# Optimization experiments

Measured on AMD Instinct MI355X. Metric: run time of the kernel, lower is better.

The kernel has to match this reference:

```python
import jax, jax.numpy as jnp
import numpy as np
from jax import lax

B, C, L = 32, 512, 2          # batch, in_channels, fcos_conv_layers
TS = (1024, 512, 256)          # temporal lengths per FPN level
STRIDES = (1, 2, 4)            # fpn_stride
EPS = 1e-5                     # BatchNorm eps (torch default)
PRIOR = 0.01                   # fcos_prior_prob


def conv1d(x, w, b, pad):
    # x: [B, Cin, T], w: [Cout, Cin, K]
    y = lax.conv_general_dilated(x, w, (1,), [(pad, pad)],
                                 dimension_numbers=('NCH', 'OIH', 'NCH'))
    return y + b[None, :, None]


def bn(x, g, be, m, v):
    # eval-mode BatchNorm1d with running stats
    s = g * lax.rsqrt(v + EPS)
    return x * s[None, :, None] + (be - m * s)[None, :, None]


def tower(x, w, b, g, be, m, v):
    # stacked [Conv1d -> BN -> ReLU] x L
    for i in range(w.shape[0]):
        x = jax.nn.relu(bn(conv1d(x, w[i], b[i], 1), g[i], be[i], m[i], v[i]))
    return x


def setup_inputs() -> dict:
    key = jax.random.key(0)
    ks = iter(jax.random.split(key, 64))

    def nrm(shape, std=0.01):
        return std * jax.random.normal(next(ks), shape, dtype=jnp.float32)

    inp = {}
    for i, t in enumerate(TS):
        inp[f'x{i}'] = jax.random.normal(next(ks), (B, C, t), dtype=jnp.float32)
    for pre in ('cls', 'box'):
        inp[pre + '_w'] = nrm((L, C, C, 3))
        inp[pre + '_b'] = jnp.zeros((L, C), jnp.float32)
        inp[pre + '_g'] = jnp.ones((L, C), jnp.float32)
        inp[pre + '_beta'] = jnp.zeros((L, C), jnp.float32)
        inp[pre + '_m'] = nrm((L, C), 0.1)
        inp[pre + '_v'] = jnp.ones((L, C), jnp.float32)
    inp['logits_w'] = nrm((1, C, 3))
    inp['logits_b'] = jnp.full((1,), -np.log((1 - PRIOR) / PRIOR), dtype=jnp.float32)
    inp['pred_w'] = nrm((2, C, 3))
    inp['pred_b'] = jnp.zeros((2,), jnp.float32)
    inp['scales'] = jnp.ones((3,), jnp.float32)
    inp['mix_w'] = nrm((C, 2 * C, 1))
    inp['mix_b'] = jnp.zeros((C,), jnp.float32)
    inp['mix_g'] = jnp.ones((C,), jnp.float32)
    inp['mix_beta'] = jnp.zeros((C,), jnp.float32)
    inp['mix_m'] = nrm((C,), 0.1)
    inp['mix_v'] = jnp.ones((C,), jnp.float32)
    H = C // 2
    inp['iou_w1'] = nrm((H, C, 3))
    inp['iou_b1'] = jnp.zeros((H,), jnp.float32)
    inp['iou_g'] = jnp.ones((H,), jnp.float32)
    inp['iou_beta'] = jnp.zeros((H,), jnp.float32)
    inp['iou_m'] = nrm((H,), 0.1)
    inp['iou_v'] = jnp.ones((H,), jnp.float32)
    inp['iou_w2'] = nrm((1, H, 1))
    inp['iou_b2'] = jnp.zeros((1,), jnp.float32)
    return inp


def _head_level(x, scale, p):
    ct = tower(x, p['cls_w'], p['cls_b'], p['cls_g'], p['cls_beta'], p['cls_m'], p['cls_v'])
    bt = tower(x, p['box_w'], p['box_b'], p['box_g'], p['box_beta'], p['box_m'], p['box_v'])
    logits = conv1d(ct, p['logits_w'], p['logits_b'], 1)                 # [B,1,T]
    bbox = jnp.exp(conv1d(bt, p['pred_w'], p['pred_b'], 1) * scale)      # [B,2,T]
    mix = jnp.concatenate([ct, bt], axis=1)                              # [B,2C,T]
    mix = jax.nn.relu(bn(conv1d(mix, p['mix_w'], p['mix_b'], 0),
                         p['mix_g'], p['mix_beta'], p['mix_m'], p['mix_v']))
    h = jax.nn.relu(bn(conv1d(mix, p['iou_w1'], p['iou_b1'], 1),
                       p['iou_g'], p['iou_beta'], p['iou_m'], p['iou_v']))
    iou = conv1d(h, p['iou_w2'], p['iou_b2'], 0)                         # [B,1,T]
    return logits, bbox, iou


def reference(x0, x1, x2, cls_w, cls_b, cls_g, cls_beta, cls_m, cls_v,
              box_w, box_b, box_g, box_beta, box_m, box_v,
              logits_w, logits_b, pred_w, pred_b, scales,
              mix_w, mix_b, mix_g, mix_beta, mix_m, mix_v,
              iou_w1, iou_b1, iou_g, iou_beta, iou_m, iou_v, iou_w2, iou_b2):
    p = dict(cls_w=cls_w, cls_b=cls_b, cls_g=cls_g, cls_beta=cls_beta, cls_m=cls_m, cls_v=cls_v,
             box_w=box_w, box_b=box_b, box_g=box_g, box_beta=box_beta, box_m=box_m, box_v=box_v,
             logits_w=logits_w, logits_b=logits_b, pred_w=pred_w, pred_b=pred_b,
             mix_w=mix_w, mix_b=mix_b, mix_g=mix_g, mix_beta=mix_beta, mix_m=mix_m, mix_v=mix_v,
             iou_w1=iou_w1, iou_b1=iou_b1, iou_g=iou_g, iou_beta=iou_beta, iou_m=iou_m, iou_v=iou_v,
             iou_w2=iou_w2, iou_b2=iou_b2)
    logits, bbox, iou = [], [], []
    for i, x in enumerate((x0, x1, x2)):
        lg, bb, io = _head_level(x, scales[i], p)
        logits.append(lg); bbox.append(bb); iou.append(io)
    # compute_locations_per_level: arange(0, t*stride, stride) + stride/2
    locs = tuple(jnp.arange(t, dtype=jnp.float32) * s + s / 2.0
                 for t, s in zip(TS, STRIDES))
    return (*logits, *bbox, *iou, *locs)
```

## Files before the change

kernel.cpp:

```cpp
#include <hip/hip_runtime.h>
#include <hip/hip_bf16.h>

typedef __hip_bfloat16 bf16;
typedef __attribute__((ext_vector_type(8))) short short8;
typedef __attribute__((ext_vector_type(4))) short short4v;
typedef __attribute__((ext_vector_type(4))) float float4v;

#define EL0 16777216ull
#define E_A0 0ull
#define E_A1 (E_A0 + EL0)
#define E_A2 (E_A1 + EL0/2)
#define E_B0 (E_A2 + EL0/4)
#define E_B1 (E_B0 + EL0)
#define E_B2 (E_B1 + EL0/2)
#define E_D0 (E_B2 + EL0/4)
#define E_W1 (E_D0 + EL0)
#define E_W2 (E_W1 + 3ull*1024*512)
#define E_WMIX (E_W2 + 3ull*1024*512)
#define E_WIOU (E_WMIX + 512ull*1024)
#define E_AFF  (E_WIOU + 3ull*256*512)

__device__ __forceinline__ void gl2lds16(const bf16* g, short* l) {
    __builtin_amdgcn_global_load_lds(
        (const __attribute__((address_space(1))) unsigned int*)g,
        (__attribute__((address_space(3))) unsigned int*)l, 16, 0, 0);
}

struct ConvP { const bf16* xa[3]; const bf16* xb[3]; const bf16* xc[3];
               bf16* ya[3]; bf16* yb[3]; };
struct HeadP { const bf16* x[3]; float* out[3]; };
struct TransP { const float* x[3]; bf16* y[3]; };
struct WSeg { const float* src; bf16* dst; int Co, Ci, K, CoTot, coOff; };
struct WP { WSeg s[6]; };
struct ASeg { const float* g; const float* be; const float* m; const float* v;
              const float* cb; float* out; int C, S; };
struct AP { ASeg s[6]; };

__global__ void wtrans_all(WP p) {
    WSeg s = p.s[blockIdx.y];
    long long n = (long long)s.Co * s.Ci * s.K;
    long long idx = (long long)blockIdx.x * 256 + threadIdx.x;
    if (idx >= n) return;
    int ci = (int)(idx % s.Ci);
    long long r = idx / s.Ci;
    int co = (int)(r % s.Co);
    int k  = (int)(r / s.Co);
    s.dst[((size_t)k * s.CoTot + s.coOff + co) * s.Ci + ci] =
        __float2bfloat16(s.src[((long long)co * s.Ci + ci) * s.K + k]);
}

__global__ void mkaff_all(AP p) {
    ASeg s = p.s[blockIdx.y];
    int i = blockIdx.x * 256 + threadIdx.x;
    if (i >= s.C) return;
    float sc = s.g[i] * rsqrtf(s.v[i] + 1e-5f);
    s.out[i] = sc;
    s.out[s.S + i] = s.cb[i] * sc + s.be[i] - s.m[i] * sc;
}

__global__ void transpose_cvt(TransP p) {
    __shared__ float tile[32][33];
    int tx = blockIdx.x;
    int lvl = (tx >= 48) ? 2 : (tx >= 32) ? 1 : 0;
    int base = (lvl == 2) ? 48 : (lvl == 1) ? 32 : 0;
    int T = 1024 >> lvl;
    int t0 = (tx - base) * 32, c0 = blockIdx.y * 32, b = blockIdx.z;
    const float* xp = p.x[lvl] + ((size_t)b * 512 + c0) * T + t0;
    for (int i = 0; i < 4; i++) {
        int c = threadIdx.y + i * 8;
        tile[c][threadIdx.x] = xp[(size_t)c * T + threadIdx.x];
    }
    __syncthreads();
    bf16* yp = p.y[lvl] + ((size_t)b * T + t0) * 512 + c0;
    for (int i = 0; i < 4; i++) {
        int t = threadIdx.y + i * 8;
        yp[(size_t)t * 512 + threadIdx.x] = __float2bfloat16(tile[threadIdx.x][t]);
    }
}

__global__ void locs_k(float* __restrict__ out) {
    int i = blockIdx.x * 256 + threadIdx.x;
    if (i < 1024)      out[i] = (float)i + 0.5f;
    else if (i < 1536) out[i] = (float)(i - 1024) * 2.0f + 1.0f;
    else if (i < 1792) out[i] = (float)(i - 1536) * 4.0f + 2.0f;
}

__global__ __launch_bounds__(256, 4) void conv_mfma(
    ConvP p, int xbsel, int xsplit, int Cin,
    const bf16* __restrict__ Wt, int taps, int CoutTot,
    const float* __restrict__ aff,
    int ybsel, int ystride, int relu)
{
    __shared__ short Alds[130 * 32];
    __shared__ short Wlds[3 * 128 * 32];

    int gy = blockIdx.y;
    int lvl = (gy >= 12) ? 2 : (gy >= 8) ? 1 : 0;
    int tb  = (lvl == 2) ? 12 : (lvl == 1) ? 8 : 0;
    int T = 1024 >> lvl;
    int t0 = (gy - tb) * 128;

    int co0 = blockIdx.x * 128, b = blockIdx.z;
    int tid = threadIdx.x;
    int lane = tid & 63, wv = tid >> 6;
    int wm = wv >> 1, wn = wv & 1;
    int quad = lane >> 4, l15 = lane & 15;
    int lr = lane >> 2, lp = lane & 3;

    const bf16* X0 = (blockIdx.x < xbsel) ? p.xa[lvl] : p.xb[lvl];
    const bf16* Xc = p.xc[lvl];

    float4v acc[4][4] = {};

    int kIters = Cin >> 5;
    int row0 = (taps == 3) ? 1 : 0;

    int pg = (lp - (lr >> 1)) & 3;
    int wslot = ((quad + (l15 >> 1)) & 3) * 8;

    for (int kk = 0; kk < kIters; kk++) {
        int ci0 = kk << 5;
        const bf16* Xk; int cl;
        if (ci0 < xsplit) { Xk = X0; cl = ci0; } else { Xk = Xc; cl = ci0 - xsplit; }
        if (kk) __syncthreads();

        for (int inst = wv; inst < 8; inst += 4) {
            int row = inst * 16 + lr;
            const bf16* g = Xk + ((size_t)b * T + t0 + row) * 512 + cl + pg * 8;
            gl2lds16(g, &Alds[(row0 + inst * 16) * 32]);
        }
        for (int inst = wv; inst < taps * 8; inst += 4) {
            int tap = inst >> 3, i2 = inst & 7;
            int row = i2 * 16 + lr;
            const bf16* g = Wt + ((size_t)tap * CoutTot + co0 + row) * Cin + ci0 + pg * 8;
            gl2lds16(g, &Wlds[tap * 4096 + i2 * 512]);
        }
        if (taps == 3 && tid < 8) {
            int top = tid >> 2;
            int h = top ? 129 : 0;
            int tg = top ? t0 + 128 : t0 - 1;
            int part = tid & 3;
            int slot = top ? part : ((part + 3) & 3);
            short8 v = {0, 0, 0, 0, 0, 0, 0, 0};
            if (tg >= 0 && tg < T)
                v = *(const short8*)(Xk + ((size_t)b * T + tg) * 512 + cl + part * 8);
            *(short8*)&Alds[h * 32 + slot * 8] = v;
        }
        __syncthreads();

        for (int tap = 0; tap < taps; tap++) {
            int aoff = ((quad + ((l15 + tap - row0) >> 1)) & 3) * 8;
            short8 af[4], bfr[4];
#pragma unroll
            for (int mi = 0; mi < 4; mi++)
                af[mi] = *(short8*)&Alds[(wm * 64 + mi * 16 + l15 + tap) * 32 + aoff];
#pragma unroll
            for (int ni = 0; ni < 4; ni++)
                bfr[ni] = *(short8*)&Wlds[tap * 4096 + (wn * 64 + ni * 16 + l15) * 32 + wslot];
#pragma unroll
            for (int mi = 0; mi < 4; mi++)
#pragma unroll
                for (int ni = 0; ni < 4; ni++)
                    acc[mi][ni] = __builtin_amdgcn_mfma_f32_16x16x32_bf16(
                        af[mi], bfr[ni], acc[mi][ni], 0, 0, 0);
        }
    }

    bf16* Yp; int colbase;
    if (blockIdx.x < ybsel) { Yp = p.ya[lvl]; colbase = co0; }
    else                    { Yp = p.yb[lvl]; colbase = co0 - 512; }
#pragma unroll
    for (int ni = 0; ni < 4; ni++) {
        int gcol = co0 + wn * 64 + ni * 16 + l15;
        int lcol = colbase + wn * 64 + ni * 16 + l15;
        float s = aff[gcol], bb = aff[CoutTot + gcol];
#pragma unroll
        for (int mi = 0; mi < 4; mi++) {
#pragma unroll
            for (int r = 0; r < 4; r++) {
                int row = t0 + wm * 64 + mi * 16 + quad * 4 + r;
                float y = acc[mi][ni][r] * s + bb;
                if (relu) y = fmaxf(y, 0.f);
                Yp[((size_t)b * T + row) * ystride + lcol] = __float2bfloat16(y);
            }
        }
    }
}

template<int CPL, int TAPS, int COUT, int MODE>
__global__ __launch_bounds__(256) void head_conv(
    HeadP p, int xstride,
    const float* __restrict__ w, const float* __restrict__ bias,
    const float* __restrict__ scale_ptr)
{
    constexpr int RW = 16;
    constexpr int Cin = CPL * 64;
    int bid = blockIdx.x;
    int lvl = (bid >= 768) ? 2 : (bid >= 512) ? 1 : 0;
    int bbase = (lvl == 2) ? 768 : (lvl == 1) ? 512 : 0;
    int T = 1024 >> lvl;
    int lane = threadIdx.x & 63, wv = threadIdx.x >> 6;
    int r0 = (bid - bbase) * 64 + wv * RW;
    int b = r0 / T, t0 = r0 - b * T;
    const bf16* base = p.x[lvl] + (size_t)b * T * xstride + lane * CPL;
    float* out = p.out[lvl];

    float wr[COUT][TAPS][CPL];
#pragma unroll
    for (int co = 0; co < COUT; co++)
#pragma unroll
        for (int k = 0; k < TAPS; k++)
#pragma unroll
            for (int j = 0; j < CPL; j++)
                wr[co][k][j] = w[((size_t)co * Cin + lane * CPL + j) * TAPS + k];
    float bia[COUT];
#pragma unroll
    for (int co = 0; co < COUT; co++) bia[co] = bias[co];
    float sc = MODE ? scale_ptr[lvl] : 0.f;

    float fprev[CPL], fcur[CPL], fnext[CPL];

    auto loadrow = [&](int t, float* f) {
        if (t < 0 || t >= T) {
#pragma unroll
            for (int j = 0; j < CPL; j++) f[j] = 0.f;
            return;
        }
        const short* q = (const short*)(base + (size_t)t * xstride);
        if constexpr (CPL == 8) {
            short8 v = *(const short8*)q;
#pragma unroll
            for (int j = 0; j < 8; j++)
                f[j] = __uint_as_float(((unsigned)(unsigned short)v[j]) << 16);
        } else {
            short4v v = *(const short4v*)q;
#pragma unroll
            for (int j = 0; j < CPL; j++)
                f[j] = __uint_as_float(((unsigned)(unsigned short)v[j]) << 16);
        }
    };

    if constexpr (TAPS == 3) { loadrow(t0 - 1, fprev); loadrow(t0, fcur); }

    for (int i = 0; i < RW; i++) {
        int t = t0 + i;
        float acc[COUT];
#pragma unroll
        for (int co = 0; co < COUT; co++) acc[co] = 0.f;
        if constexpr (TAPS == 3) {
            loadrow(t + 1, fnext);
#pragma unroll
            for (int co = 0; co < COUT; co++)
#pragma unroll
                for (int j = 0; j < CPL; j++)
                    acc[co] += fprev[j] * wr[co][0][j] + fcur[j] * wr[co][1][j]
                             + fnext[j] * wr[co][2][j];
#pragma unroll
            for (int j = 0; j < CPL; j++) { fprev[j] = fcur[j]; fcur[j] = fnext[j]; }
        } else {
            loadrow(t, fcur);
#pragma unroll
            for (int co = 0; co < COUT; co++)
#pragma unroll
                for (int j = 0; j < CPL; j++)
                    acc[co] += fcur[j] * wr[co][0][j];
        }
#pragma unroll
        for (int co = 0; co < COUT; co++)
#pragma unroll
            for (int off = 32; off; off >>= 1)
                acc[co] += __shfl_down(acc[co], off);
        if (lane == 0) {
#pragma unroll
            for (int co = 0; co < COUT; co++) {
                float v = acc[co] + bia[co];
                if (MODE) v = expf(v * sc);
                out[((size_t)b * COUT + co) * T + t] = v;
            }
        }
    }
}

extern "C" void kernel_launch(void* const* d_in, const int* in_sizes, int n_in,
                              void* d_out, int out_size, void* d_ws, size_t ws_size,
                              hipStream_t stream) {
    const float* xin0 = (const float*)d_in[0];
    const float* xin1 = (const float*)d_in[1];
    const float* xin2 = (const float*)d_in[2];
    const float* cls_w  = (const float*)d_in[3];
    const float* cls_b  = (const float*)d_in[4];
    const float* cls_g  = (const float*)d_in[5];
    const float* cls_be = (const float*)d_in[6];
    const float* cls_m  = (const float*)d_in[7];
    const float* cls_v  = (const float*)d_in[8];
    const float* box_w  = (const float*)d_in[9];
    const float* box_b  = (const float*)d_in[10];
    const float* box_g  = (const float*)d_in[11];
    const float* box_be = (const float*)d_in[12];
    const float* box_m  = (const float*)d_in[13];
    const float* box_v  = (const float*)d_in[14];
    const float* logits_w = (const float*)d_in[15];
    const float* logits_b = (const float*)d_in[16];
    const float* pred_w   = (const float*)d_in[17];
    const float* pred_b   = (const float*)d_in[18];
    const float* scales   = (const float*)d_in[19];
    const float* mix_w  = (const float*)d_in[20];
    const float* mix_b  = (const float*)d_in[21];
    const float* mix_g  = (const float*)d_in[22];
    const float* mix_be = (const float*)d_in[23];
    const float* mix_m  = (const float*)d_in[24];
    const float* mix_v  = (const float*)d_in[25];
    const float* iou_w1 = (const float*)d_in[26];
    const float* iou_b1 = (const float*)d_in[27];
    const float* iou_g  = (const float*)d_in[28];
    const float* iou_be = (const float*)d_in[29];
    const float* iou_m  = (const float*)d_in[30];
    const float* iou_v  = (const float*)d_in[31];
    const float* iou_w2 = (const float*)d_in[32];
    const float* iou_b2 = (const float*)d_in[33];

    float* out = (float*)d_out;
    bf16* wsb = (bf16*)d_ws;

    bf16* A[3] = { wsb + E_A0, wsb + E_A1, wsb + E_A2 };
    bf16* Bb[3] = { wsb + E_B0, wsb + E_B1, wsb + E_B2 };
    bf16* C[3] = { (bf16*)xin0, (bf16*)xin0 + EL0, (bf16*)xin0 + EL0 + EL0/2 };
    bf16* D[3] = { wsb + E_D0, (bf16*)xin1, (bf16*)xin1 + EL0/2 };
    bf16* W1   = wsb + E_W1;
    bf16* W2   = wsb + E_W2;
    bf16* WMIX = wsb + E_WMIX;
    bf16* WIOU = wsb + E_WIOU;
    float* AFF = (float*)(wsb + E_AFF);

    const int BIG = 1 << 30;
    const int WL = 512 * 512 * 3;

    {
        WP wp;
        wp.s[0] = { cls_w,      W1, 512, 512, 3, 1024, 0 };
        wp.s[1] = { box_w,      W1, 512, 512, 3, 1024, 512 };
        wp.s[2] = { cls_w + WL, W2, 512, 512, 3, 1024, 0 };
        wp.s[3] = { box_w + WL, W2, 512, 512, 3, 1024, 512 };
        wp.s[4] = { mix_w,  WMIX, 512, 1024, 1, 512, 0 };
        wp.s[5] = { iou_w1, WIOU, 256, 512, 3, 256, 0 };
        wtrans_all<<<dim3(3072, 6), 256, 0, stream>>>(wp);

        AP ap;
        ap.s[0] = { cls_g,       cls_be,       cls_m,       cls_v,       cls_b,       AFF + 0,          512, 1024 };
        ap.s[1] = { box_g,       box_be,       box_m,       box_v,       box_b,       AFF + 512,        512, 1024 };
        ap.s[2] = { cls_g + 512, cls_be + 512, cls_m + 512, cls_v + 512, cls_b + 512, AFF + 2048,       512, 1024 };
        ap.s[3] = { box_g + 512, box_be + 512, box_m + 512, box_v + 512, box_b + 512, AFF + 2048 + 512, 512, 1024 };
        ap.s[4] = { mix_g, mix_be, mix_m, mix_v, mix_b,  AFF + 4096, 512, 512 };
        ap.s[5] = { iou_g, iou_be, iou_m, iou_v, iou_b1, AFF + 5120, 256, 256 };
        mkaff_all<<<dim3(2, 6), 256, 0, stream>>>(ap);

        locs_k<<<7, 256, 0, stream>>>(out + 229376);
    }

    float* LOG[3] = { out + 0,      out + 32768,  out + 49152 };
    float* BBX[3] = { out + 57344,  out + 122880, out + 155648 };
    float* IOU[3] = { out + 172032, out + 204800, out + 221184 };

    {
        TransP tp;
        tp.x[0] = xin0; tp.x[1] = xin1; tp.x[2] = xin2;
        tp.y[0] = A[0]; tp.y[1] = A[1]; tp.y[2] = A[2];
        transpose_cvt<<<dim3(56, 16, 32), dim3(32, 8), 0, stream>>>(tp);
    }

    {
        ConvP cp;
        for (int l = 0; l < 3; l++) {
            cp.xa[l] = A[l]; cp.xb[l] = A[l]; cp.xc[l] = A[l];
            cp.ya[l] = Bb[l]; cp.yb[l] = C[l];
        }
        conv_mfma<<<dim3(8, 14, 32), 256, 0, stream>>>(
            cp, 8, BIG, 512, W1, 3, 1024, AFF + 0, 4, 512, 1);
    }
    {
        ConvP cp;
        for (int l = 0; l < 3; l++) {
            cp.xa[l] = Bb[l]; cp.xb[l] = C[l]; cp.xc[l] = Bb[l];
            cp.ya[l] = D[l]; cp.yb[l] = A[l];
        }
        conv_mfma<<<dim3(8, 14, 32), 256, 0, stream>>>(
            cp, 4, BIG, 512, W2, 3, 1024, AFF + 2048, 4, 512, 1);
    }
    {
        HeadP hp;
        for (int l = 0; l < 3; l++) { hp.x[l] = D[l]; hp.out[l] = LOG[l]; }
        head_conv<8, 3, 1, 0><<<896, 256, 0, stream>>>(hp, 512, logits_w, logits_b, scales);
        HeadP hp2;
        for (int l = 0; l < 3; l++) { hp2.x[l] = A[l]; hp2.out[l] = BBX[l]; }
        head_conv<8, 3, 2, 1><<<896, 256, 0, stream>>>(hp2, 512, pred_w, pred_b, scales);
    }
    {
        ConvP cp;
        for (int l = 0; l < 3; l++) {
            cp.xa[l] = D[l]; cp.xb[l] = D[l]; cp.xc[l] = A[l];
            cp.ya[l] = Bb[l]; cp.yb[l] = Bb[l];
        }
        conv_mfma<<<dim3(4, 14, 32), 256, 0, stream>>>(
            cp, 8, 512, 1024, WMIX, 1, 512, AFF + 4096, 8, 512, 1);
    }
    {
        ConvP cp;
        for (int l = 0; l < 3; l++) {
            cp.xa[l] = Bb[l]; cp.xb[l] = Bb[l]; cp.xc[l] = Bb[l];
            cp.ya[l] = C[l]; cp.yb[l] = C[l];
        }
        conv_mfma<<<dim3(2, 14, 32), 256, 0, stream>>>(
            cp, 8, BIG, 512, WIOU, 3, 256, AFF + 5120, 8, 256, 1);
    }
    {
        HeadP hp;
        for (int l = 0; l < 3; l++) { hp.x[l] = C[l]; hp.out[l] = IOU[l]; }
        head_conv<4, 1, 1, 0><<<896, 256, 0, stream>>>(hp, 256, iou_w2, iou_b2, scales);
    }
}
```

Before: 770.7 us.

## Fuse all stages into one persistent cooperative kernel with grid syncs

Replaces the chain of separate launches (weight transpose, affine prep, locs, input transpose, four convs, three heads) with a single persistent cooperative kernel that loops over work units and separates dependent stages with grid.sync. The logits and bbox heads now run in the same phase as the mix conv instead of as separate launches. The aim is to remove launch overhead and inter-kernel gaps. In exchange the persistent grid is capped by occupancy, so each block processes many tiles serially, and every grid-wide barrier costs time. A fallback multi-kernel path is kept in case the cooperative launch fails.

```diff
diff --git a/kernel.cpp b/kernel.cpp
--- a/kernel.cpp
+++ b/kernel.cpp
@@ -1,4 +1,5 @@
 #include <hip/hip_runtime.h>
+#include <hip/hip_cooperative_groups.h>
 #include <hip/hip_bf16.h>
 
 typedef __hip_bfloat16 bf16;
@@ -26,95 +27,54 @@
         (__attribute__((address_space(3))) unsigned int*)l, 16, 0, 0);
 }
 
-struct ConvP { const bf16* xa[3]; const bf16* xb[3]; const bf16* xc[3];
-               bf16* ya[3]; bf16* yb[3]; };
-struct HeadP { const bf16* x[3]; float* out[3]; };
-struct TransP { const float* x[3]; bf16* y[3]; };
 struct WSeg { const float* src; bf16* dst; int Co, Ci, K, CoTot, coOff; };
-struct WP { WSeg s[6]; };
 struct ASeg { const float* g; const float* be; const float* m; const float* v;
               const float* cb; float* out; int C, S; };
-struct AP { ASeg s[6]; };
-
-__global__ void wtrans_all(WP p) {
-    WSeg s = p.s[blockIdx.y];
-    long long n = (long long)s.Co * s.Ci * s.K;
-    long long idx = (long long)blockIdx.x * 256 + threadIdx.x;
-    if (idx >= n) return;
-    int ci = (int)(idx % s.Ci);
-    long long r = idx / s.Ci;
-    int co = (int)(r % s.Co);
-    int k  = (int)(r / s.Co);
-    s.dst[((size_t)k * s.CoTot + s.coOff + co) * s.Ci + ci] =
-        __float2bfloat16(s.src[((long long)co * s.Ci + ci) * s.K + k]);
-}
-
-__global__ void mkaff_all(AP p) {
-    ASeg s = p.s[blockIdx.y];
-    int i = blockIdx.x * 256 + threadIdx.x;
-    if (i >= s.C) return;
-    float sc = s.g[i] * rsqrtf(s.v[i] + 1e-5f);
-    s.out[i] = sc;
-    s.out[s.S + i] = s.cb[i] * sc + s.be[i] - s.m[i] * sc;
-}
-
-__global__ void transpose_cvt(TransP p) {
-    __shared__ float tile[32][33];
-    int tx = blockIdx.x;
-    int lvl = (tx >= 48) ? 2 : (tx >= 32) ? 1 : 0;
-    int base = (lvl == 2) ? 48 : (lvl == 1) ? 32 : 0;
-    int T = 1024 >> lvl;
-    int t0 = (tx - base) * 32, c0 = blockIdx.y * 32, b = blockIdx.z;
-    const float* xp = p.x[lvl] + ((size_t)b * 512 + c0) * T + t0;
-    for (int i = 0; i < 4; i++) {
-        int c = threadIdx.y + i * 8;
-        tile[c][threadIdx.x] = xp[(size_t)c * T + threadIdx.x];
-    }
-    __syncthreads();
-    bf16* yp = p.y[lvl] + ((size_t)b * T + t0) * 512 + c0;
-    for (int i = 0; i < 4; i++) {
-        int t = threadIdx.y + i * 8;
-        yp[(size_t)t * 512 + threadIdx.x] = __float2bfloat16(tile[threadIdx.x][t]);
-    }
-}
-
-__global__ void locs_k(float* __restrict__ out) {
-    int i = blockIdx.x * 256 + threadIdx.x;
-    if (i < 1024)      out[i] = (float)i + 0.5f;
-    else if (i < 1536) out[i] = (float)(i - 1024) * 2.0f + 1.0f;
-    else if (i < 1792) out[i] = (float)(i - 1536) * 4.0f + 2.0f;
-}
-
-__global__ __launch_bounds__(256, 4) void conv_mfma(
-    ConvP p, int xbsel, int xsplit, int Cin,
+struct MegaP {
+    WSeg wseg[6];
+    ASeg aseg[6];
+    const float* tx[3]; bf16* ty[3];
+    const bf16* c1xa[3]; const bf16* c1xb[3]; const bf16* c1xc[3]; bf16* c1ya[3]; bf16* c1yb[3];
+    const bf16* c2xa[3]; const bf16* c2xb[3]; const bf16* c2xc[3]; bf16* c2ya[3]; bf16* c2yb[3];
+    const bf16* mxa[3];  const bf16* mxb[3];  const bf16* mxc[3];  bf16* mya[3];  bf16* myb[3];
+    const bf16* ixa[3];  const bf16* ixb[3];  const bf16* ixc[3];  bf16* iya[3];  bf16* iyb[3];
+    const bf16 *W1, *W2, *WMIX, *WIOU;
+    const float* AFF;
+    const bf16* hL[3]; float* oL[3];
+    const bf16* hP[3]; float* oP[3];
+    const bf16* hI[3]; float* oI[3];
+    const float *logits_w, *logits_b, *pred_w, *pred_b, *scales, *iou_w2, *iou_b2;
+    float* locs;
+};
+
+__device__ __forceinline__ void conv_tile(
+    int bx, int gy, int b,
+    const bf16* const* Xav, const bf16* const* Xbv, int xbsel,
+    const bf16* const* Xcv, int xsplit, int Cin,
     const bf16* __restrict__ Wt, int taps, int CoutTot,
     const float* __restrict__ aff,
-    int ybsel, int ystride, int relu)
+    bf16* const* Yav, bf16* const* Ybv, int ybsel, int ystride,
+    short* Alds, short* Wlds)
 {
-    __shared__ short Alds[130 * 32];
-    __shared__ short Wlds[3 * 128 * 32];
-
-    int gy = blockIdx.y;
     int lvl = (gy >= 12) ? 2 : (gy >= 8) ? 1 : 0;
     int tb  = (lvl == 2) ? 12 : (lvl == 1) ? 8 : 0;
     int T = 1024 >> lvl;
     int t0 = (gy - tb) * 128;
 
-    int co0 = blockIdx.x * 128, b = blockIdx.z;
+    int co0 = bx * 128;
     int tid = threadIdx.x;
     int lane = tid & 63, wv = tid >> 6;
     int wm = wv >> 1, wn = wv & 1;
     int quad = lane >> 4, l15 = lane & 15;
     int lr = lane >> 2, lp = lane & 3;
 
-    const bf16* X0 = (blockIdx.x < xbsel) ? p.xa[lvl] : p.xb[lvl];
-    const bf16* Xc = p.xc[lvl];
+    const bf16* X0 = (bx < xbsel) ? Xav[lvl] : Xbv[lvl];
+    const bf16* Xc = Xcv[lvl];
 
     float4v acc[4][4] = {};
 
     int kIters = Cin >> 5;
     int row0 = (taps == 3) ? 1 : 0;
-
     int pg = (lp - (lr >> 1)) & 3;
     int wslot = ((quad + (l15 >> 1)) & 3) * 8;
 
@@ -122,7 +82,7 @@
         int ci0 = kk << 5;
         const bf16* Xk; int cl;
         if (ci0 < xsplit) { Xk = X0; cl = ci0; } else { Xk = Xc; cl = ci0 - xsplit; }
-        if (kk) __syncthreads();
+        __syncthreads();
 
         for (int inst = wv; inst < 8; inst += 4) {
             int row = inst * 16 + lr;
@@ -167,8 +127,8 @@
     }
 
     bf16* Yp; int colbase;
-    if (blockIdx.x < ybsel) { Yp = p.ya[lvl]; colbase = co0; }
-    else                    { Yp = p.yb[lvl]; colbase = co0 - 512; }
+    if (bx < ybsel) { Yp = Yav[lvl]; colbase = co0; }
+    else            { Yp = Ybv[lvl]; colbase = co0 - 512; }
 #pragma unroll
     for (int ni = 0; ni < 4; ni++) {
         int gcol = co0 + wn * 64 + ni * 16 + l15;
@@ -180,7 +140,7 @@
             for (int r = 0; r < 4; r++) {
                 int row = t0 + wm * 64 + mi * 16 + quad * 4 + r;
                 float y = acc[mi][ni][r] * s + bb;
-                if (relu) y = fmaxf(y, 0.f);
+                y = fmaxf(y, 0.f);
                 Yp[((size_t)b * T + row) * ystride + lcol] = __float2bfloat16(y);
             }
         }
@@ -188,22 +148,21 @@
 }
 
 template<int CPL, int TAPS, int COUT, int MODE>
-__global__ __launch_bounds__(256) void head_conv(
-    HeadP p, int xstride,
+__device__ __forceinline__ void head_unit(
+    int unit, const bf16* const* Xv, int xstride,
     const float* __restrict__ w, const float* __restrict__ bias,
-    const float* __restrict__ scale_ptr)
+    const float* __restrict__ scale_ptr, float* const* outv)
 {
     constexpr int RW = 16;
     constexpr int Cin = CPL * 64;
-    int bid = blockIdx.x;
-    int lvl = (bid >= 768) ? 2 : (bid >= 512) ? 1 : 0;
+    int lvl = (unit >= 768) ? 2 : (unit >= 512) ? 1 : 0;
     int bbase = (lvl == 2) ? 768 : (lvl == 1) ? 512 : 0;
     int T = 1024 >> lvl;
-    int lane = threadIdx.x & 63, wv = threadIdx.x >> 6;
-    int r0 = (bid - bbase) * 64 + wv * RW;
+    int lane = threadIdx.x & 63, wvv = threadIdx.x >> 6;
+    int r0 = (unit - bbase) * 64 + wvv * RW;
     int b = r0 / T, t0 = r0 - b * T;
-    const bf16* base = p.x[lvl] + (size_t)b * T * xstride + lane * CPL;
-    float* out = p.out[lvl];
+    const bf16* base = Xv[lvl] + (size_t)b * T * xstride + lane * CPL;
+    float* out = outv[lvl];
 
     float wr[COUT][TAPS][CPL];
 #pragma unroll
@@ -219,7 +178,6 @@
     float sc = MODE ? scale_ptr[lvl] : 0.f;
 
     float fprev[CPL], fcur[CPL], fnext[CPL];
-
     auto loadrow = [&](int t, float* f) {
         if (t < 0 || t >= T) {
 #pragma unroll
@@ -279,6 +237,152 @@
             }
         }
     }
+}
+
+__device__ __forceinline__ void transpose_tile(int u, const float* const* xv,
+                                               bf16* const* yv, float* ttile)
+{
+    int bx = u % 56, rest = u / 56;
+    int cy = rest & 15, b = rest >> 4;
+    int lvl = (bx >= 48) ? 2 : (bx >= 32) ? 1 : 0;
+    int base = (lvl == 2) ? 48 : (lvl == 1) ? 32 : 0;
+    int T = 1024 >> lvl;
+    int t0 = (bx - base) * 32, c0 = cy * 32;
+    int tx = threadIdx.x & 31, ty = threadIdx.x >> 5;
+    const float* xp = xv[lvl] + ((size_t)b * 512 + c0) * T + t0;
+    for (int i = 0; i < 4; i++) {
+        int c = ty + i * 8;
+        ttile[c * 33 + tx] = xp[(size_t)c * T + tx];
+    }
+    __syncthreads();
+    bf16* yp = yv[lvl] + ((size_t)b * T + t0) * 512 + c0;
+    for (int i = 0; i < 4; i++) {
+        int t = ty + i * 8;
+        yp[(size_t)t * 512 + tx] = __float2bfloat16(ttile[tx * 33 + t]);
+    }
+}
+
+__device__ __forceinline__ void prep_body(const MegaP& p, unsigned bid, unsigned nb) {
+    int tid = threadIdx.x;
+    for (int s = 0; s < 6; s++) {
+        WSeg w = p.wseg[s];
+        long long n = (long long)w.Co * w.Ci * w.K;
+        for (long long i = (long long)bid * 256 + tid; i < n; i += (long long)nb * 256) {
+            int ci = (int)(i % w.Ci);
+            long long r = i / w.Ci;
+            int co = (int)(r % w.Co);
+            int k  = (int)(r / w.Co);
+            w.dst[((size_t)k * w.CoTot + w.coOff + co) * w.Ci + ci] =
+                __float2bfloat16(w.src[((long long)co * w.Ci + ci) * w.K + k]);
+        }
+    }
+    for (int s = 0; s < 6; s++) {
+        ASeg a = p.aseg[s];
+        for (int i = bid * 256 + tid; i < a.C; i += nb * 256) {
+            float sc = a.g[i] * rsqrtf(a.v[i] + 1e-5f);
+            a.out[i] = sc;
+            a.out[a.S + i] = a.cb[i] * sc + a.be[i] - a.m[i] * sc;
+        }
+    }
+    for (int i = bid * 256 + tid; i < 1792; i += nb * 256) {
+        float v;
+        if (i < 1024)      v = (float)i + 0.5f;
+        else if (i < 1536) v = (float)(i - 1024) * 2.0f + 1.0f;
+        else               v = (float)(i - 1536) * 4.0f + 2.0f;
+        p.locs[i] = v;
+    }
+}
+
+__global__ __launch_bounds__(256, 4) void mega(MegaP p) {
+    __shared__ short smem[16448];
+    short* Alds = smem;
+    short* Wlds = smem + 4160;
+    float* ttile = (float*)smem;
+
+    auto grid = cooperative_groups::this_grid();
+    unsigned nb = gridDim.x, bid = blockIdx.x;
+    const int BIGS = 1 << 30;
+
+    prep_body(p, bid, nb);
+    for (unsigned u = bid; u < 28672; u += nb) {
+        transpose_tile(u, p.tx, p.ty, ttile);
+        __syncthreads();
+    }
+    grid.sync();
+
+    for (unsigned u = bid; u < 3584; u += nb) {
+        int bx = u & 7, r = u >> 3, gy = r % 14, b = r / 14;
+        conv_tile(bx, gy, b, p.c1xa, p.c1xb, 8, p.c1xc, BIGS, 512,
+                  p.W1, 3, 1024, p.AFF + 0, p.c1ya, p.c1yb, 4, 512, Alds, Wlds);
+    }
+    grid.sync();
+
+    for (unsigned u = bid; u < 3584; u += nb) {
+        int bx = u & 7, r = u >> 3, gy = r % 14, b = r / 14;
+        conv_tile(bx, gy, b, p.c2xa, p.c2xb, 4, p.c2xc, BIGS, 512,
+                  p.W2, 3, 1024, p.AFF + 2048, p.c2ya, p.c2yb, 4, 512, Alds, Wlds);
+    }
+    grid.sync();
+
+    for (unsigned u = bid; u < 3584; u += nb) {
+        if (u < 1792) {
+            int bx = u & 3, r = u >> 2, gy = r % 14, b = r / 14;
+            conv_tile(bx, gy, b, p.mxa, p.mxb, 4, p.mxc, 512, 1024,
+                      p.WMIX, 1, 512, p.AFF + 4096, p.mya, p.myb, 8, 512, Alds, Wlds);
+        } else if (u < 2688) {
+            head_unit<8, 3, 1, 0>(u - 1792, p.hL, 512, p.logits_w, p.logits_b, p.scales, p.oL);
+        } else {
+            head_unit<8, 3, 2, 1>(u - 2688, p.hP, 512, p.pred_w, p.pred_b, p.scales, p.oP);
+        }
+    }
+    grid.sync();
+
+    for (unsigned u = bid; u < 896; u += nb) {
+        int bx = u & 1, r = u >> 1, gy = r % 14, b = r / 14;
+        conv_tile(bx, gy, b, p.ixa, p.ixb, 2, p.ixc, BIGS, 512,
+                  p.WIOU, 3, 256, p.AFF + 5120, p.iya, p.iyb, 2, 256, Alds, Wlds);
+    }
+    grid.sync();
+
+    for (unsigned u = bid; u < 896; u += nb) {
+        head_unit<4, 1, 1, 0>(u, p.hI, 256, p.iou_w2, p.iou_b2, p.scales, p.oI);
+    }
+}
+
+__global__ __launch_bounds__(256) void prep_k(MegaP p) {
+    prep_body(p, blockIdx.x, gridDim.x);
+}
+
+__global__ __launch_bounds__(256) void trans_k(MegaP p) {
+    __shared__ float ttile[32 * 33];
+    transpose_tile(blockIdx.x, p.tx, p.ty, ttile);
+}
+
+__global__ __launch_bounds__(256, 4) void conv_k(MegaP p, int which) {
+    __shared__ short smem[16448];
+    short* Alds = smem;
+    short* Wlds = smem + 4160;
+    const int BIGS = 1 << 30;
+    int bx = blockIdx.x, gy = blockIdx.y, b = blockIdx.z;
+    if (which == 0)
+        conv_tile(bx, gy, b, p.c1xa, p.c1xb, 8, p.c1xc, BIGS, 512,
+                  p.W1, 3, 1024, p.AFF + 0, p.c1ya, p.c1yb, 4, 512, Alds, Wlds);
+    else if (which == 1)
+        conv_tile(bx, gy, b, p.c2xa, p.c2xb, 4, p.c2xc, BIGS, 512,
+                  p.W2, 3, 1024, p.AFF + 2048, p.c2ya, p.c2yb, 4, 512, Alds, Wlds);
+    else if (which == 2)
+        conv_tile(bx, gy, b, p.mxa, p.mxb, 4, p.mxc, 512, 1024,
+                  p.WMIX, 1, 512, p.AFF + 4096, p.mya, p.myb, 8, 512, Alds, Wlds);
+    else
+        conv_tile(bx, gy, b, p.ixa, p.ixb, 2, p.ixc, BIGS, 512,
+                  p.WIOU, 3, 256, p.AFF + 5120, p.iya, p.iyb, 2, 256, Alds, Wlds);
+}
+
+__global__ __launch_bounds__(256) void head_k(MegaP p, int which) {
+    int u = blockIdx.x;
+    if (which == 0)      head_unit<8, 3, 1, 0>(u, p.hL, 512, p.logits_w, p.logits_b, p.scales, p.oL);
+    else if (which == 1) head_unit<8, 3, 2, 1>(u, p.hP, 512, p.pred_w, p.pred_b, p.scales, p.oP);
+    else                 head_unit<4, 1, 1, 0>(u, p.hI, 256, p.iou_w2, p.iou_b2, p.scales, p.oI);
 }
 
 extern "C" void kernel_launch(void* const* d_in, const int* in_sizes, int n_in,
@@ -332,89 +436,65 @@
     bf16* WIOU = wsb + E_WIOU;
     float* AFF = (float*)(wsb + E_AFF);
 
-    const int BIG = 1 << 30;
     const int WL = 512 * 512 * 3;
 
-    {
-        WP wp;
-        wp.s[0] = { cls_w,      W1, 512, 512, 3, 1024, 0 };
-        wp.s[1] = { box_w,      W1, 512, 512, 3, 1024, 512 };
-        wp.s[2] = { cls_w + WL, W2, 512, 512, 3, 1024, 0 };
-        wp.s[3] = { box_w + WL, W2, 512, 512, 3, 1024, 512 };
-        wp.s[4] = { mix_w,  WMIX, 512, 1024, 1, 512, 0 };
-        wp.s[5] = { iou_w1, WIOU, 256, 512, 3, 256, 0 };
-        wtrans_all<<<dim3(3072, 6), 256, 0, stream>>>(wp);
-
-        AP ap;
-        ap.s[0] = { cls_g,       cls_be,       cls_m,       cls_v,       cls_b,       AFF + 0,          512, 1024 };
-        ap.s[1] = { box_g,       box_be,       box_m,       box_v,       box_b,       AFF + 512,        512, 1024 };
-        ap.s[2] = { cls_g + 512, cls_be + 512, cls_m + 512, cls_v + 512, cls_b + 512, AFF + 2048,       512, 1024 };
-        ap.s[3] = { box_g + 512, box_be + 512, box_m + 512, box_v + 512, box_b + 512, AFF + 2048 + 512, 512, 1024 };
-        ap.s[4] = { mix_g, mix_be, mix_m, mix_v, mix_b,  AFF + 4096, 512, 512 };
-        ap.s[5] = { iou_g, iou_be, iou_m, iou_v, iou_b1, AFF + 5120, 256, 256 };
-        mkaff_all<<<dim3(2, 6), 256, 0, stream>>>(ap);
-
-        locs_k<<<7, 256, 0, stream>>>(out + 229376);
-    }
-
-    float* LOG[3] = { out + 0,      out + 32768,  out + 49152 };
-    float* BBX[3] = { out + 57344,  out + 122880, out + 155648 };
-    float* IOU[3] = { out + 172032, out + 204800, out + 221184 };
-
-    {
-        TransP tp;
-        tp.x[0] = xin0; tp.x[1] = xin1; tp.x[2] = xin2;
-        tp.y[0] = A[0]; tp.y[1] = A[1]; tp.y[2] = A[2];
-        transpose_cvt<<<dim3(56, 16, 32), dim3(32, 8), 0, stream>>>(tp);
-    }
-
-    {
-        ConvP cp;
-        for (int l = 0; l < 3; l++) {
-            cp.xa[l] = A[l]; cp.xb[l] = A[l]; cp.xc[l] = A[l];
-            cp.ya[l] = Bb[l]; cp.yb[l] = C[l];
-        }
-        conv_mfma<<<dim3(8, 14, 32), 256, 0, stream>>>(
-            cp, 8, BIG, 512, W1, 3, 1024, AFF + 0, 4, 512, 1);
-    }
-    {
-        ConvP cp;
-        for (int l = 0; l < 3; l++) {
-            cp.xa[l] = Bb[l]; cp.xb[l] = C[l]; cp.xc[l] = Bb[l];
-            cp.ya[l] = D[l]; cp.yb[l] = A[l];
-        }
-        conv_mfma<<<dim3(8, 14, 32), 256, 0, stream>>>(
-            cp, 4, BIG, 512, W2, 3, 1024, AFF + 2048, 4, 512, 1);
-    }
-    {
-        HeadP hp;
-        for (int l = 0; l < 3; l++) { hp.x[l] = D[l]; hp.out[l] = LOG[l]; }
-        head_conv<8, 3, 1, 0><<<896, 256, 0, stream>>>(hp, 512, logits_w, logits_b, scales);
-        HeadP hp2;
-        for (int l = 0; l < 3; l++) { hp2.x[l] = A[l]; hp2.out[l] = BBX[l]; }
-        head_conv<8, 3, 2, 1><<<896, 256, 0, stream>>>(hp2, 512, pred_w, pred_b, scales);
-    }
-    {
-        ConvP cp;
-        for (int l = 0; l < 3; l++) {
-            cp.xa[l] = D[l]; cp.xb[l] = D[l]; cp.xc[l] = A[l];
-            cp.ya[l] = Bb[l]; cp.yb[l] = Bb[l];
-        }
-        conv_mfma<<<dim3(4, 14, 32), 256, 0, stream>>>(
-            cp, 8, 512, 1024, WMIX, 1, 512, AFF + 4096, 8, 512, 1);
-    }
-    {
-        ConvP cp;
-        for (int l = 0; l < 3; l++) {
-            cp.xa[l] = Bb[l]; cp.xb[l] = Bb[l]; cp.xc[l] = Bb[l];
-            cp.ya[l] = C[l]; cp.yb[l] = C[l];
-        }
-        conv_mfma<<<dim3(2, 14, 32), 256, 0, stream>>>(
-            cp, 8, BIG, 512, WIOU, 3, 256, AFF + 5120, 8, 256, 1);
-    }
-    {
-        HeadP hp;
-        for (int l = 0; l < 3; l++) { hp.x[l] = C[l]; hp.out[l] = IOU[l]; }
-        head_conv<4, 1, 1, 0><<<896, 256, 0, stream>>>(hp, 256, iou_w2, iou_b2, scales);
-    }
-}
+    MegaP p;
+    p.wseg[0] = { cls_w,      W1, 512, 512, 3, 1024, 0 };
+    p.wseg[1] = { box_w,      W1, 512, 512, 3, 1024, 512 };
+    p.wseg[2] = { cls_w + WL, W2, 512, 512, 3, 1024, 0 };
+    p.wseg[3] = { box_w + WL, W2, 512, 512, 3, 1024, 512 };
+    p.wseg[4] = { mix_w,  WMIX, 512, 1024, 1, 512, 0 };
+    p.wseg[5] = { iou_w1, WIOU, 256, 512, 3, 256, 0 };
+    p.aseg[0] = { cls_g,       cls_be,       cls_m,       cls_v,       cls_b,       AFF + 0,          512, 1024 };
+    p.aseg[1] = { box_g,       box_be,       box_m,       box_v,       box_b,       AFF + 512,        512, 1024 };
+    p.aseg[2] = { cls_g + 512, cls_be + 512, cls_m + 512, cls_v + 512, cls_b + 512, AFF + 2048,       512, 1024 };
+    p.aseg[3] = { box_g + 512, box_be + 512, box_m + 512, box_v + 512, box_b + 512, AFF + 2048 + 512, 512, 1024 };
+    p.aseg[4] = { mix_g, mix_be, mix_m, mix_v, mix_b,  AFF + 4096, 512, 512 };
+    p.aseg[5] = { iou_g, iou_be, iou_m, iou_v, iou_b1, AFF + 5120, 256, 256 };
+
+    p.tx[0] = xin0; p.tx[1] = xin1; p.tx[2] = xin2;
+    for (int l = 0; l < 3; l++) {
+        p.ty[l] = A[l];
+        p.c1xa[l] = A[l]; p.c1xb[l] = A[l]; p.c1xc[l] = A[l];
+        p.c1ya[l] = Bb[l]; p.c1yb[l] = C[l];
+        p.c2xa[l] = Bb[l]; p.c2xb[l] = C[l]; p.c2xc[l] = Bb[l];
+        p.c2ya[l] = D[l]; p.c2yb[l] = A[l];
+        p.mxa[l] = D[l]; p.mxb[l] = D[l]; p.mxc[l] = A[l];
+        p.mya[l] = Bb[l]; p.myb[l] = Bb[l];
+        p.ixa[l] = Bb[l]; p.ixb[l] = Bb[l]; p.ixc[l] = Bb[l];
+        p.iya[l] = C[l]; p.iyb[l] = C[l];
+        p.hL[l] = D[l]; p.hP[l] = A[l]; p.hI[l] = C[l];
+    }
+    p.W1 = W1; p.W2 = W2; p.WMIX = WMIX; p.WIOU = WIOU; p.AFF = AFF;
+    p.oL[0] = out + 0;      p.oL[1] = out + 32768;  p.oL[2] = out + 49152;
+    p.oP[0] = out + 57344;  p.oP[1] = out + 122880; p.oP[2] = out + 155648;
+    p.oI[0] = out + 172032; p.oI[1] = out + 204800; p.oI[2] = out + 221184;
+    p.logits_w = logits_w; p.logits_b = logits_b;
+    p.pred_w = pred_w; p.pred_b = pred_b; p.scales = scales;
+    p.iou_w2 = iou_w2; p.iou_b2 = iou_b2;
+    p.locs = out + 229376;
+
+    hipError_t st = hipErrorUnknown;
+    int dev = 0, nCU = 0, occ = 0;
+    if (hipGetDevice(&dev) == hipSuccess &&
+        hipDeviceGetAttribute(&nCU, hipDeviceAttributeMultiprocessorCount, dev) == hipSuccess &&
+        hipOccupancyMaxActiveBlocksPerMultiprocessor(&occ, (const void*)mega, 256, 0) == hipSuccess &&
+        occ >= 1 && nCU >= 1) {
+        unsigned grid = (unsigned)occ * (unsigned)nCU;
+        if (grid > 1024) grid = 1024;
+        void* args[] = { &p };
+        st = hipLaunchCooperativeKernel((const void*)mega, dim3(grid), dim3(256),
+                                        args, 0u, stream);
+    }
+    if (st != hipSuccess) {
+        prep_k<<<512, 256, 0, stream>>>(p);
+        trans_k<<<28672, 256, 0, stream>>>(p);
+        conv_k<<<dim3(8, 14, 32), 256, 0, stream>>>(p, 0);
+        conv_k<<<dim3(8, 14, 32), 256, 0, stream>>>(p, 1);
+        head_k<<<896, 256, 0, stream>>>(p, 0);
+        head_k<<<896, 256, 0, stream>>>(p, 1);
+        conv_k<<<dim3(4, 14, 32), 256, 0, stream>>>(p, 2);
+        conv_k<<<dim3(2, 14, 32), 256, 0, stream>>>(p, 3);
+        head_k<<<896, 256, 0, stream>>>(p, 2);
+    }
+}
```

Measured after the change: 1.232 ms. 59.8% more time.
